# Kernel optimization log

Measured on AMD Instinct MI355X. Metric: run time of the kernel, lower is better.

The kernel has to match this reference:

```python
import jax, jax.numpy as jnp
import numpy as np

N = 500_000   # total nodes
B = 4096      # number of graphs (segments)
D = 256       # feature dim (input_dim)
H = 4         # attention heads


def setup_inputs() -> dict:
    key = jax.random.key(0)
    ks = jax.random.split(key, 9)
    x = jax.random.normal(ks[0], (N, D), dtype=jnp.float32)
    membership = jnp.sort(jax.random.randint(ks[1], (N,), 0, B, dtype=jnp.int32))
    # xavier-normal-ish attention weight, shape (1, H, D//H)
    att_w = jax.random.normal(ks[2], (1, H, D // H), dtype=jnp.float32) * np.float32(np.sqrt(2.0 / (1 + D // H)))
    s = np.float32(1.0 / np.sqrt(D))
    gru_w_ih = jax.random.uniform(ks[3], (3 * D, D), minval=-s, maxval=s, dtype=jnp.float32)
    gru_w_hh = jax.random.uniform(ks[4], (3 * D, D), minval=-s, maxval=s, dtype=jnp.float32)
    gru_b_ih = jax.random.uniform(ks[5], (3 * D,), minval=-s, maxval=s, dtype=jnp.float32)
    gru_b_hh = jax.random.uniform(ks[6], (3 * D,), minval=-s, maxval=s, dtype=jnp.float32)
    sm = np.float32(1.0 / np.sqrt(4 * D))
    merge_w = jax.random.uniform(ks[7], (D, 4 * D), minval=-sm, maxval=sm, dtype=jnp.float32)
    merge_b = jax.random.uniform(ks[8], (D,), minval=-sm, maxval=sm, dtype=jnp.float32)
    return {"x": x, "membership": membership, "att_w": att_w,
            "gru_w_ih": gru_w_ih, "gru_w_hh": gru_w_hh,
            "gru_b_ih": gru_b_ih, "gru_b_hh": gru_b_hh,
            "merge_w": merge_w, "merge_b": merge_b}


def _readout(x, seg, att_w, gru_w_ih, gru_w_hh, gru_b_ih, gru_b_hh, merge_w, merge_b):
    n, d = x.shape
    # ---- branch 0: 'rnn-sum-max' (GRUCell on pseudo-nodes) ----
    h = jax.nn.gelu(x, approximate=False)                       # exact gelu as torch F.gelu
    center = jax.ops.segment_sum(h, seg, num_segments=B)        # op_center = 'sum'  (B, D)
    neighbor = jax.ops.segment_max(h, seg, num_segments=B)      # op_neighbor = 'max' (B, D)
    gi = center @ gru_w_ih.T + gru_b_ih                          # (B, 3D)
    gh = neighbor @ gru_w_hh.T + gru_b_hh                        # (B, 3D)
    i_r, i_z, i_n = jnp.split(gi, 3, axis=-1)
    h_r, h_z, h_n = jnp.split(gh, 3, axis=-1)
    r = jax.nn.sigmoid(i_r + h_r)
    z = jax.nn.sigmoid(i_z + h_z)
    ng = jnp.tanh(i_n + r * h_n)
    rnn_out = (1.0 - z) * ng + z * neighbor                      # (B, D)
    # ---- branch 1: 'att' (single mode, segment softmax) ----
    xv = x.reshape(n, H, d // H)
    alpha = jax.nn.leaky_relu(jnp.sum(xv * att_w, axis=-1), negative_slope=0.2)  # (N, H)
    amax = jax.ops.segment_max(alpha, seg, num_segments=B)       # (B, H)
    e = jnp.exp(alpha - amax[seg])
    denom = jax.ops.segment_sum(e, seg, num_segments=B)
    a = e / denom[seg]                                           # segment softmax (N, H)
    att_out = jax.ops.segment_sum((xv * a[:, :, None]).reshape(n, d), seg, num_segments=B)
    # ---- branch 2/3: 'max', 'sum' ----
    max_out = jax.ops.segment_max(x, seg, num_segments=B)
    sum_out = jax.ops.segment_sum(x, seg, num_segments=B)
    # ---- merge: cat + Linear ----
    merged = jnp.concatenate([rnn_out, att_out, max_out, sum_out], axis=-1)  # (B, 4D)
    return merged @ merge_w.T + merge_b                          # (B, D)


def reference(x, membership, att_w, gru_w_ih, gru_w_hh, gru_b_ih, gru_b_hh, merge_w, merge_b):
    return _readout(x, membership, att_w, gru_w_ih, gru_w_hh, gru_b_ih, gru_b_hh, merge_w, merge_b)
```

## Files before the change

### kernel.cpp

```cpp
#include <hip/hip_runtime.h>
#include <math.h>
#include <stdint.h>

#define NN 500000
#define NB 4096
#define DD 256
#define NBND 1954
#define WPREP 640

typedef short  short8  __attribute__((ext_vector_type(8)));
typedef short  short4v __attribute__((ext_vector_type(4)));
typedef float  floatx4 __attribute__((ext_vector_type(4)));
typedef float  f2      __attribute__((ext_vector_type(2)));

__device__ __forceinline__ f2 sp(float v) { return (f2){v, v}; }

__device__ __forceinline__ short f2bf(float f) {
    uint32_t u = __float_as_uint(f);
    u += 0x7fffu + ((u >> 16) & 1u);
    return (short)(u >> 16);
}
__device__ __forceinline__ float bf2f(short s) {
    uint32_t u = ((uint32_t)(unsigned short)s) << 16;
    return __uint_as_float(u);
}

__device__ __forceinline__ f2 gelu2(f2 x) {
    f2 z = __builtin_elementwise_abs(x) * sp(0.70710678118654752440f);
    f2 p = __builtin_elementwise_fma(z, sp(0.0000430638f), sp(0.0002765672f));
    p = __builtin_elementwise_fma(p, z, sp(0.0001520143f));
    p = __builtin_elementwise_fma(p, z, sp(0.0092705272f));
    p = __builtin_elementwise_fma(p, z, sp(0.0422820123f));
    p = __builtin_elementwise_fma(p, z, sp(0.0705230784f));
    p = __builtin_elementwise_fma(p, z, sp(1.0f));
    p = p * p; p = p * p; p = p * p; p = p * p;
    f2 r = { __builtin_amdgcn_rcpf(p.x), __builtin_amdgcn_rcpf(p.y) };
    f2 er = __builtin_elementwise_copysign(sp(1.0f) - r, x);
    return sp(0.5f) * x * (sp(1.0f) + er);
}

__global__ __launch_bounds__(256) void prep_kernel(
    const int*   __restrict__ seg,
    const float* __restrict__ w_ih,
    const float* __restrict__ w_hh,
    const float* __restrict__ merge_w,
    int*   __restrict__ bnd,
    short* __restrict__ wih_bf,
    short* __restrict__ whh_bf,
    short* __restrict__ mw_bf)
{
    const int bid = blockIdx.x;
    const int t   = threadIdx.x;
    if (bid < NBND) {
        int i = bid * 256 + t;
        if (i >= NN) return;
        int s = seg[i];
        if (i == 0) {
            for (int b = 0; b <= s; ++b) bnd[b] = 0;
        } else {
            int p = seg[i - 1];
            for (int b = p + 1; b <= s; ++b) bnd[b] = i;
        }
        if (i == NN - 1) {
            for (int b = s + 1; b <= NB; ++b) bnd[b] = NN;
        }
    } else {
        int base = (bid - NBND) * 1024 + t * 4;
        const float* src; short* dst;
        if (base < 196608)      { src = &w_ih[base];            dst = &wih_bf[base]; }
        else if (base < 393216) { src = &w_hh[base - 196608];   dst = &whh_bf[base - 196608]; }
        else                    { src = &merge_w[base - 393216]; dst = &mw_bf[base - 393216]; }
        float4 v = *(const float4*)src;
        *(short4v*)dst = (short4v){ f2bf(v.x), f2bf(v.y), f2bf(v.z), f2bf(v.w) };
    }
}

__global__ __launch_bounds__(256, 8) void seg_kernel(
    const float* __restrict__ x,
    const int*   __restrict__ bnd,
    const float* __restrict__ att_w,
    short* __restrict__ merged_bf,
    short* __restrict__ center_bf,
    short* __restrict__ neighbor_bf)
{
    const int b   = blockIdx.x;
    const int tid = threadIdx.x;
    const int w   = tid >> 6;
    const int l   = tid & 63;

    const int start = bnd[b];
    const int end   = bnd[b + 1];

    const int cnt = end - start;
    const int q = cnt >> 2, r = cnt & 3;
    const int my_start = start + w * q + (w < r ? w : r);
    const int my_cnt   = q + (w < r ? 1 : 0);

    const float4 awv = *reinterpret_cast<const float4*>(&att_w[4 * l]);
    const f2 aw01 = {awv.x, awv.y}, aw23 = {awv.z, awv.w};

    f2 c01 = sp(0.f), c23 = sp(0.f);
    f2 s01 = sp(0.f), s23 = sp(0.f);
    f2 m01 = sp(-INFINITY), m23 = sp(-INFINITY);
    f2 a01 = sp(0.f), a23 = sp(0.f);
    float lsum = 0.f;

    auto process = [&](const float4& v) {
        f2 vl = {v.x, v.y}, vh = {v.z, v.w};
        f2 gl = gelu2(vl), gh = gelu2(vh);
        c01 += gl; c23 += gh;
        s01 += vl; s23 += vh;
        m01 = __builtin_elementwise_max(m01, vl);
        m23 = __builtin_elementwise_max(m23, vh);
        f2 tp = __builtin_elementwise_fma(vh, aw23, vl * aw01);
        float t = tp.x + tp.y;
        t += __shfl_xor(t, 1, 64);
        t += __shfl_xor(t, 2, 64);
        t += __shfl_xor(t, 4, 64);
        t += __shfl_xor(t, 8, 64);
        float alpha = fmaxf(t, 0.2f * t);
        float e = __expf(alpha);
        lsum += e;
        f2 ev = sp(e);
        a01 = __builtin_elementwise_fma(ev, vl, a01);
        a23 = __builtin_elementwise_fma(ev, vh, a23);
    };

    const float* __restrict__ xl = x + 4 * l;
    auto LD = [&](int row) -> float4 {
        int rc = row < (NN - 1) ? row : (NN - 1);
        return *reinterpret_cast<const float4*>(&xl[(size_t)rc * DD]);
    };

    float4 q0 = LD(my_start),     q1 = LD(my_start + 1),
           q2 = LD(my_start + 2), q3 = LD(my_start + 3);
    int ip = my_start + 4;
    int rem = my_cnt;
    while (rem >= 2) {
        float4 f0 = LD(ip), f1 = LD(ip + 1);
        process(q0); process(q1);
        q0 = q2; q1 = q3; q2 = f0; q3 = f1;
        ip += 2; rem -= 2;
    }
    if (rem) process(q0);

    __shared__ float lds[4][4][256];
    __shared__ float ldsl[4][4];
    const int c = 4 * l;
    lds[0][w][c+0] = c01.x; lds[0][w][c+1] = c01.y; lds[0][w][c+2] = c23.x; lds[0][w][c+3] = c23.y;
    lds[1][w][c+0] = s01.x; lds[1][w][c+1] = s01.y; lds[1][w][c+2] = s23.x; lds[1][w][c+3] = s23.y;
    lds[2][w][c+0] = m01.x; lds[2][w][c+1] = m01.y; lds[2][w][c+2] = m23.x; lds[2][w][c+3] = m23.y;
    lds[3][w][c+0] = a01.x; lds[3][w][c+1] = a01.y; lds[3][w][c+2] = a23.x; lds[3][w][c+3] = a23.y;
    if ((l & 15) == 0) ldsl[w][l >> 4] = lsum;
    __syncthreads();

    const int d = tid;
    float cs = lds[0][0][d] + lds[0][1][d] + lds[0][2][d] + lds[0][3][d];
    float ss = lds[1][0][d] + lds[1][1][d] + lds[1][2][d] + lds[1][3][d];
    float mm = fmaxf(fmaxf(lds[2][0][d], lds[2][1][d]), fmaxf(lds[2][2][d], lds[2][3][d]));
    float ac = lds[3][0][d] + lds[3][1][d] + lds[3][2][d] + lds[3][3][d];
    const int h = d >> 6;
    float denom = ldsl[0][h] + ldsl[1][h] + ldsl[2][h] + ldsl[3][h];
    float att = (denom > 0.f) ? ac / denom : 0.f;
    float nm = gelu2((f2){mm, mm}).x;

    short* mrow = merged_bf + (size_t)b * 1024;
    mrow[256 + d] = f2bf(att);
    mrow[512 + d] = f2bf(mm);
    mrow[768 + d] = f2bf(ss);
    center_bf  [(size_t)b * DD + d] = f2bf(cs);
    neighbor_bf[(size_t)b * DD + d] = f2bf(nm);
}

__global__ __launch_bounds__(256) void gru_and_basemerge(
    const short* __restrict__ center_bf,
    const short* __restrict__ neighbor_bf,
    const short* __restrict__ wih_bf,
    const short* __restrict__ whh_bf,
    const float* __restrict__ b_ih,
    const float* __restrict__ b_hh,
    short* __restrict__ merged_bf,
    const short* __restrict__ mw_bf,
    const float* __restrict__ merge_b,
    float* __restrict__ out)
{
    __shared__ short smem[16128];
    const int t   = threadIdx.x;
    const int w   = t >> 6, l = t & 63;
    const int l15 = l & 15, lq = l >> 4;

    if (blockIdx.x < 1024) {
        short* Ac = smem;
        short* An = smem + 4608;
        short* Wt = smem + 9216;

        const int m0 = (blockIdx.x >> 4) * 64;
        const int j0 = (blockIdx.x & 15) * 16;
        const int lr = t >> 2;
        const int lc = (t & 3) * 16;

        int wg[3], wrow[3], wk8[3];
        const short* wbase[3];
        #pragma unroll
        for (int i = 0; i < 3; ++i) {
            int f = i * 256 + t;
            wg[i]  = f >> 7;
            int idx = f & 127;
            wrow[i] = idx >> 3;
            wk8[i]  = (idx & 7) * 8;
            wbase[i] = (wg[i] < 3)
                ? &wih_bf[(size_t)(wg[i] * 256 + j0 + wrow[i]) * 256 + wk8[i]]
                : &whh_bf[(size_t)((wg[i] - 3) * 256 + j0 + wrow[i]) * 256 + wk8[i]];
        }
        const short* crp = &center_bf  [(size_t)(m0 + lr) * 256 + lc];
        const short* nrp = &neighbor_bf[(size_t)(m0 + lr) * 256 + lc];

        floatx4 acc[6] = {};

        short8 c0 = *(const short8*)(crp), c1 = *(const short8*)(crp + 8);
        short8 n0 = *(const short8*)(nrp), n1 = *(const short8*)(nrp + 8);
        short8 wv0 = *(const short8*)(wbase[0]);
        short8 wv1 = *(const short8*)(wbase[1]);
        short8 wv2 = *(const short8*)(wbase[2]);

        for (int k0 = 0; k0 < 256; k0 += 64) {
            const int kn = (k0 + 64 < 256) ? k0 + 64 : k0;
            short8 nc0 = *(const short8*)(crp + kn), nc1 = *(const short8*)(crp + kn + 8);
            short8 nn0 = *(const short8*)(nrp + kn), nn1 = *(const short8*)(nrp + kn + 8);
            short8 nw0 = *(const short8*)(wbase[0] + kn);
            short8 nw1 = *(const short8*)(wbase[1] + kn);
            short8 nw2 = *(const short8*)(wbase[2] + kn);

            __syncthreads();
            *(short8*)&Ac[lr * 72 + lc]     = c0;
            *(short8*)&Ac[lr * 72 + lc + 8] = c1;
            *(short8*)&An[lr * 72 + lc]     = n0;
            *(short8*)&An[lr * 72 + lc + 8] = n1;
            *(short8*)&Wt[wg[0] * 1152 + wrow[0] * 72 + wk8[0]] = wv0;
            *(short8*)&Wt[wg[1] * 1152 + wrow[1] * 72 + wk8[1]] = wv1;
            *(short8*)&Wt[wg[2] * 1152 + wrow[2] * 72 + wk8[2]] = wv2;
            __syncthreads();

            short8 afc[2], afn[2];
            #pragma unroll
            for (int ks = 0; ks < 2; ++ks) {
                afc[ks] = *(short8*)&Ac[(w * 16 + l15) * 72 + ks * 32 + lq * 8];
                afn[ks] = *(short8*)&An[(w * 16 + l15) * 72 + ks * 32 + lq * 8];
            }
            #pragma unroll
            for (int gg = 0; gg < 6; ++gg) {
                #pragma unroll
                for (int ks = 0; ks < 2; ++ks) {
                    short8 bf = *(short8*)&Wt[gg * 1152 + l15 * 72 + ks * 32 + lq * 8];
                    acc[gg] = __builtin_amdgcn_mfma_f32_16x16x32_bf16(
                        (gg < 3) ? afc[ks] : afn[ks], bf, acc[gg], 0, 0, 0);
                }
            }

            c0 = nc0; c1 = nc1; n0 = nn0; n1 = nn1;
            wv0 = nw0; wv1 = nw1; wv2 = nw2;
        }

        const int col = j0 + l15;
        const float bir = b_ih[col], biz = b_ih[256 + col], bin = b_ih[512 + col];
        const float bhr = b_hh[col], bhz = b_hh[256 + col], bhn = b_hh[512 + col];
        #pragma unroll
        for (int qq = 0; qq < 4; ++qq) {
            const int row = m0 + w * 16 + lq * 4 + qq;
            float rr = 1.f / (1.f + __expf(-(acc[0][qq] + bir + acc[3][qq] + bhr)));
            float zz = 1.f / (1.f + __expf(-(acc[1][qq] + biz + acc[4][qq] + bhz)));
            float ng = tanhf(acc[2][qq] + bin + rr * (acc[5][qq] + bhn));
            float nb = bf2f(neighbor_bf[(size_t)row * 256 + col]);
            merged_bf[(size_t)row * 1024 + col] = f2bf((1.f - zz) * ng + zz * nb);
        }
    } else {
        short* As = smem;
        short* Bs = smem + 4608;

        const int bid2 = blockIdx.x - 1024;
        const int m0 = (bid2 & 63) * 64, n0 = (bid2 >> 6) * 64;
        const int arow = t >> 2, ak = (t & 3) * 16;
        const int wm = w >> 1, wn = w & 1;

        const short* ap = &merged_bf[(size_t)(m0 + arow) * 1024 + 256 + ak];
        const short* bp = &mw_bf    [(size_t)(n0 + arow) * 1024 + 256 + ak];

        floatx4 acc[2][2] = {};

        short8 a0 = *(const short8*)(ap), a1 = *(const short8*)(ap + 8);
        short8 b0 = *(const short8*)(bp), b1 = *(const short8*)(bp + 8);

        for (int k0 = 0; k0 < 768; k0 += 64) {
            const int kn = (k0 + 64 < 768) ? k0 + 64 : k0;
            short8 na0 = *(const short8*)(ap + kn), na1 = *(const short8*)(ap + kn + 8);
            short8 nb0 = *(const short8*)(bp + kn), nb1 = *(const short8*)(bp + kn + 8);

            __syncthreads();
            *(short8*)&As[arow * 72 + ak]     = a0;
            *(short8*)&As[arow * 72 + ak + 8] = a1;
            *(short8*)&Bs[arow * 72 + ak]     = b0;
            *(short8*)&Bs[arow * 72 + ak + 8] = b1;
            __syncthreads();

            #pragma unroll
            for (int ks = 0; ks < 2; ++ks) {
                short8 af0 = *(short8*)&As[(wm * 32 +      l15) * 72 + ks * 32 + lq * 8];
                short8 af1 = *(short8*)&As[(wm * 32 + 16 + l15) * 72 + ks * 32 + lq * 8];
                short8 bf0 = *(short8*)&Bs[(wn * 32 +      l15) * 72 + ks * 32 + lq * 8];
                short8 bf1 = *(short8*)&Bs[(wn * 32 + 16 + l15) * 72 + ks * 32 + lq * 8];
                acc[0][0] = __builtin_amdgcn_mfma_f32_16x16x32_bf16(af0, bf0, acc[0][0], 0, 0, 0);
                acc[0][1] = __builtin_amdgcn_mfma_f32_16x16x32_bf16(af0, bf1, acc[0][1], 0, 0, 0);
                acc[1][0] = __builtin_amdgcn_mfma_f32_16x16x32_bf16(af1, bf0, acc[1][0], 0, 0, 0);
                acc[1][1] = __builtin_amdgcn_mfma_f32_16x16x32_bf16(af1, bf1, acc[1][1], 0, 0, 0);
            }

            a0 = na0; a1 = na1; b0 = nb0; b1 = nb1;
        }

        #pragma unroll
        for (int mi = 0; mi < 2; ++mi) {
            #pragma unroll
            for (int nj = 0; nj < 2; ++nj) {
                const int col = n0 + wn * 32 + 16 * nj + l15;
                const float bv = merge_b[col];
                #pragma unroll
                for (int qq = 0; qq < 4; ++qq) {
                    const int row = m0 + wm * 32 + 16 * mi + lq * 4 + qq;
                    out[(size_t)row * 256 + col] = acc[mi][nj][qq] + bv;
                }
            }
        }
    }
}

__global__ __launch_bounds__(256) void rnn_merge(
    const short* __restrict__ merged_bf,
    const short* __restrict__ mw_bf,
    float* __restrict__ out)
{
    __shared__ short As[64 * 72];
    __shared__ short Bs[64 * 72];

    const int t   = threadIdx.x;
    const int w   = t >> 6, l = t & 63;
    const int wm  = w >> 1, wn = w & 1;
    const int m0  = (blockIdx.x & 63) * 64, n0 = (blockIdx.x >> 6) * 64;
    const int arow = t >> 2, ak = (t & 3) * 16;
    const int l15 = l & 15, lq = l >> 4;

    const short* ap = &merged_bf[(size_t)(m0 + arow) * 1024 + ak];
    const short* bp = &mw_bf    [(size_t)(n0 + arow) * 1024 + ak];

    floatx4 acc[2][2] = {};

    short8 a0 = *(const short8*)(ap), a1 = *(const short8*)(ap + 8);
    short8 b0 = *(const short8*)(bp), b1 = *(const short8*)(bp + 8);

    for (int k0 = 0; k0 < 256; k0 += 64) {
        const int kn = (k0 + 64 < 256) ? k0 + 64 : k0;
        short8 na0 = *(const short8*)(ap + kn), na1 = *(const short8*)(ap + kn + 8);
        short8 nb0 = *(const short8*)(bp + kn), nb1 = *(const short8*)(bp + kn + 8);

        __syncthreads();
        *(short8*)&As[arow * 72 + ak]     = a0;
        *(short8*)&As[arow * 72 + ak + 8] = a1;
        *(short8*)&Bs[arow * 72 + ak]     = b0;
        *(short8*)&Bs[arow * 72 + ak + 8] = b1;
        __syncthreads();

        #pragma unroll
        for (int ks = 0; ks < 2; ++ks) {
            short8 af0 = *(short8*)&As[(wm * 32 +      l15) * 72 + ks * 32 + lq * 8];
            short8 af1 = *(short8*)&As[(wm * 32 + 16 + l15) * 72 + ks * 32 + lq * 8];
            short8 bf0 = *(short8*)&Bs[(wn * 32 +      l15) * 72 + ks * 32 + lq * 8];
            short8 bf1 = *(short8*)&Bs[(wn * 32 + 16 + l15) * 72 + ks * 32 + lq * 8];
            acc[0][0] = __builtin_amdgcn_mfma_f32_16x16x32_bf16(af0, bf0, acc[0][0], 0, 0, 0);
            acc[0][1] = __builtin_amdgcn_mfma_f32_16x16x32_bf16(af0, bf1, acc[0][1], 0, 0, 0);
            acc[1][0] = __builtin_amdgcn_mfma_f32_16x16x32_bf16(af1, bf0, acc[1][0], 0, 0, 0);
            acc[1][1] = __builtin_amdgcn_mfma_f32_16x16x32_bf16(af1, bf1, acc[1][1], 0, 0, 0);
        }

        a0 = na0; a1 = na1; b0 = nb0; b1 = nb1;
    }

    #pragma unroll
    for (int mi = 0; mi < 2; ++mi) {
        #pragma unroll
        for (int nj = 0; nj < 2; ++nj) {
            const int col = n0 + wn * 32 + 16 * nj + l15;
            #pragma unroll
            for (int qq = 0; qq < 4; ++qq) {
                const int row = m0 + wm * 32 + 16 * mi + lq * 4 + qq;
                out[(size_t)row * 256 + col] += acc[mi][nj][qq];
            }
        }
    }
}

extern "C" void kernel_launch(void* const* d_in, const int* in_sizes, int n_in,
                              void* d_out, int out_size, void* d_ws, size_t ws_size,
                              hipStream_t stream) {
    const float* x       = (const float*)d_in[0];
    const int*   seg     = (const int*)  d_in[1];
    const float* att_w   = (const float*)d_in[2];
    const float* w_ih    = (const float*)d_in[3];
    const float* w_hh    = (const float*)d_in[4];
    const float* b_ih    = (const float*)d_in[5];
    const float* b_hh    = (const float*)d_in[6];
    const float* merge_w = (const float*)d_in[7];
    const float* merge_b = (const float*)d_in[8];
    float* out = (float*)d_out;

    short* merged_bf   = (short*)d_ws;
    short* center_bf   = merged_bf   + (size_t)NB * 1024;
    short* neighbor_bf = center_bf   + (size_t)NB * DD;
    int*   bnd         = (int*)(neighbor_bf + (size_t)NB * DD);
    short* wih_bf      = (short*)(bnd + 8192);
    short* whh_bf      = wih_bf + 196608;
    short* mw_bf       = whh_bf + 196608;

    prep_kernel<<<NBND + WPREP, 256, 0, stream>>>(
        seg, w_ih, w_hh, merge_w, bnd, wih_bf, whh_bf, mw_bf);

    seg_kernel<<<NB, 256, 0, stream>>>(x, bnd, att_w, merged_bf, center_bf, neighbor_bf);

    gru_and_basemerge<<<1024 + 256, 256, 0, stream>>>(
        center_bf, neighbor_bf, wih_bf, whh_bf, b_ih, b_hh,
        merged_bf, mw_bf, merge_b, out);

    rnn_merge<<<256, 256, 0, stream>>>(merged_bf, mw_bf, out);
}
```

Before: 135.0 us.

## Move weight bf16 conversion into seg kernel and halve rnn_merge M-tile

The fp32-to-bf16 weight conversion blocks move out of the prep kernel and are appended as extra blocks to the segment reduction kernel, leaving a small boundary-only kernel in front. The conversion then overlaps with the bandwidth-heavy segment pass and shortens the dependency chain before it. Separately, the rnn_merge GEMM tile shrinks from 64x64 to 32x64, doubling the block count to 512 for better CU coverage on a small GEMM, at the cost of more B-tile reloads per output.

```diff
diff --git a/kernel.cpp b/kernel.cpp
--- a/kernel.cpp
+++ b/kernel.cpp
@@ -39,52 +39,51 @@
     return sp(0.5f) * x * (sp(1.0f) + er);
 }
 
-__global__ __launch_bounds__(256) void prep_kernel(
-    const int*   __restrict__ seg,
+__global__ __launch_bounds__(256) void seg_bounds(
+    const int* __restrict__ seg, int* __restrict__ bnd)
+{
+    int i = blockIdx.x * 256 + threadIdx.x;
+    if (i >= NN) return;
+    int s = seg[i];
+    if (i == 0) {
+        for (int b = 0; b <= s; ++b) bnd[b] = 0;
+    } else {
+        int p = seg[i - 1];
+        for (int b = p + 1; b <= s; ++b) bnd[b] = i;
+    }
+    if (i == NN - 1) {
+        for (int b = s + 1; b <= NB; ++b) bnd[b] = NN;
+    }
+}
+
+__global__ __launch_bounds__(256, 8) void seg_kernel(
+    const float* __restrict__ x,
+    const int*   __restrict__ bnd,
+    const float* __restrict__ att_w,
     const float* __restrict__ w_ih,
     const float* __restrict__ w_hh,
     const float* __restrict__ merge_w,
-    int*   __restrict__ bnd,
+    short* __restrict__ merged_bf,
+    short* __restrict__ center_bf,
+    short* __restrict__ neighbor_bf,
     short* __restrict__ wih_bf,
     short* __restrict__ whh_bf,
     short* __restrict__ mw_bf)
 {
-    const int bid = blockIdx.x;
-    const int t   = threadIdx.x;
-    if (bid < NBND) {
-        int i = bid * 256 + t;
-        if (i >= NN) return;
-        int s = seg[i];
-        if (i == 0) {
-            for (int b = 0; b <= s; ++b) bnd[b] = 0;
-        } else {
-            int p = seg[i - 1];
-            for (int b = p + 1; b <= s; ++b) bnd[b] = i;
-        }
-        if (i == NN - 1) {
-            for (int b = s + 1; b <= NB; ++b) bnd[b] = NN;
-        }
-    } else {
-        int base = (bid - NBND) * 1024 + t * 4;
+    const int tid = threadIdx.x;
+
+    if (blockIdx.x >= NB) {
+        int base = (blockIdx.x - NB) * 1024 + tid * 4;
         const float* src; short* dst;
-        if (base < 196608)      { src = &w_ih[base];            dst = &wih_bf[base]; }
-        else if (base < 393216) { src = &w_hh[base - 196608];   dst = &whh_bf[base - 196608]; }
+        if (base < 196608)      { src = &w_ih[base];             dst = &wih_bf[base]; }
+        else if (base < 393216) { src = &w_hh[base - 196608];    dst = &whh_bf[base - 196608]; }
         else                    { src = &merge_w[base - 393216]; dst = &mw_bf[base - 393216]; }
         float4 v = *(const float4*)src;
         *(short4v*)dst = (short4v){ f2bf(v.x), f2bf(v.y), f2bf(v.z), f2bf(v.w) };
-    }
-}
-
-__global__ __launch_bounds__(256, 8) void seg_kernel(
-    const float* __restrict__ x,
-    const int*   __restrict__ bnd,
-    const float* __restrict__ att_w,
-    short* __restrict__ merged_bf,
-    short* __restrict__ center_bf,
-    short* __restrict__ neighbor_bf)
-{
+        return;
+    }
+
     const int b   = blockIdx.x;
-    const int tid = threadIdx.x;
     const int w   = tid >> 6;
     const int l   = tid & 63;
 
@@ -338,61 +337,55 @@
     const short* __restrict__ mw_bf,
     float* __restrict__ out)
 {
-    __shared__ short As[64 * 72];
+    __shared__ short As[32 * 72];
     __shared__ short Bs[64 * 72];
 
     const int t   = threadIdx.x;
     const int w   = t >> 6, l = t & 63;
     const int wm  = w >> 1, wn = w & 1;
-    const int m0  = (blockIdx.x & 63) * 64, n0 = (blockIdx.x >> 6) * 64;
-    const int arow = t >> 2, ak = (t & 3) * 16;
+    const int m0  = (blockIdx.x & 127) * 32, n0 = (blockIdx.x >> 7) * 64;
+    const int arow = t >> 3, ak = (t & 7) * 8;
+    const int brow = t >> 2, bk = (t & 3) * 16;
     const int l15 = l & 15, lq = l >> 4;
 
     const short* ap = &merged_bf[(size_t)(m0 + arow) * 1024 + ak];
-    const short* bp = &mw_bf    [(size_t)(n0 + arow) * 1024 + ak];
-
-    floatx4 acc[2][2] = {};
-
-    short8 a0 = *(const short8*)(ap), a1 = *(const short8*)(ap + 8);
+    const short* bp = &mw_bf    [(size_t)(n0 + brow) * 1024 + bk];
+
+    floatx4 acc[2] = {};
+
+    short8 a0 = *(const short8*)(ap);
     short8 b0 = *(const short8*)(bp), b1 = *(const short8*)(bp + 8);
 
     for (int k0 = 0; k0 < 256; k0 += 64) {
         const int kn = (k0 + 64 < 256) ? k0 + 64 : k0;
-        short8 na0 = *(const short8*)(ap + kn), na1 = *(const short8*)(ap + kn + 8);
+        short8 na0 = *(const short8*)(ap + kn);
         short8 nb0 = *(const short8*)(bp + kn), nb1 = *(const short8*)(bp + kn + 8);
 
         __syncthreads();
-        *(short8*)&As[arow * 72 + ak]     = a0;
-        *(short8*)&As[arow * 72 + ak + 8] = a1;
-        *(short8*)&Bs[arow * 72 + ak]     = b0;
-        *(short8*)&Bs[arow * 72 + ak + 8] = b1;
+        *(short8*)&As[arow * 72 + ak]    = a0;
+        *(short8*)&Bs[brow * 72 + bk]    = b0;
+        *(short8*)&Bs[brow * 72 + bk + 8] = b1;
         __syncthreads();
 
         #pragma unroll
         for (int ks = 0; ks < 2; ++ks) {
-            short8 af0 = *(short8*)&As[(wm * 32 +      l15) * 72 + ks * 32 + lq * 8];
-            short8 af1 = *(short8*)&As[(wm * 32 + 16 + l15) * 72 + ks * 32 + lq * 8];
+            short8 af  = *(short8*)&As[(wm * 16 + l15) * 72 + ks * 32 + lq * 8];
             short8 bf0 = *(short8*)&Bs[(wn * 32 +      l15) * 72 + ks * 32 + lq * 8];
             short8 bf1 = *(short8*)&Bs[(wn * 32 + 16 + l15) * 72 + ks * 32 + lq * 8];
-            acc[0][0] = __builtin_amdgcn_mfma_f32_16x16x32_bf16(af0, bf0, acc[0][0], 0, 0, 0);
-            acc[0][1] = __builtin_amdgcn_mfma_f32_16x16x32_bf16(af0, bf1, acc[0][1], 0, 0, 0);
-            acc[1][0] = __builtin_amdgcn_mfma_f32_16x16x32_bf16(af1, bf0, acc[1][0], 0, 0, 0);
-            acc[1][1] = __builtin_amdgcn_mfma_f32_16x16x32_bf16(af1, bf1, acc[1][1], 0, 0, 0);
-        }
-
-        a0 = na0; a1 = na1; b0 = nb0; b1 = nb1;
+            acc[0] = __builtin_amdgcn_mfma_f32_16x16x32_bf16(af, bf0, acc[0], 0, 0, 0);
+            acc[1] = __builtin_amdgcn_mfma_f32_16x16x32_bf16(af, bf1, acc[1], 0, 0, 0);
+        }
+
+        a0 = na0; b0 = nb0; b1 = nb1;
     }
 
     #pragma unroll
-    for (int mi = 0; mi < 2; ++mi) {
+    for (int nj = 0; nj < 2; ++nj) {
+        const int col = n0 + wn * 32 + 16 * nj + l15;
         #pragma unroll
-        for (int nj = 0; nj < 2; ++nj) {
-            const int col = n0 + wn * 32 + 16 * nj + l15;
-            #pragma unroll
-            for (int qq = 0; qq < 4; ++qq) {
-                const int row = m0 + wm * 32 + 16 * mi + lq * 4 + qq;
-                out[(size_t)row * 256 + col] += acc[mi][nj][qq];
-            }
+        for (int qq = 0; qq < 4; ++qq) {
+            const int row = m0 + wm * 16 + lq * 4 + qq;
+            out[(size_t)row * 256 + col] += acc[nj][qq];
         }
     }
 }
@@ -419,14 +412,15 @@
     short* whh_bf      = wih_bf + 196608;
     short* mw_bf       = whh_bf + 196608;
 
-    prep_kernel<<<NBND + WPREP, 256, 0, stream>>>(
-        seg, w_ih, w_hh, merge_w, bnd, wih_bf, whh_bf, mw_bf);
-
-    seg_kernel<<<NB, 256, 0, stream>>>(x, bnd, att_w, merged_bf, center_bf, neighbor_bf);
+    seg_bounds<<<NBND, 256, 0, stream>>>(seg, bnd);
+
+    seg_kernel<<<NB + WPREP, 256, 0, stream>>>(
+        x, bnd, att_w, w_ih, w_hh, merge_w,
+        merged_bf, center_bf, neighbor_bf, wih_bf, whh_bf, mw_bf);
 
     gru_and_basemerge<<<1024 + 256, 256, 0, stream>>>(
         center_bf, neighbor_bf, wih_bf, whh_bf, b_ih, b_hh,
         merged_bf, mw_bf, merge_b, out);
 
-    rnn_merge<<<256, 256, 0, stream>>>(merged_bf, mw_bf, out);
-}
+    rnn_merge<<<512, 256, 0, stream>>>(merged_bf, mw_bf, out);
+}
```

New measurement: 133.3 us. Within noise of the previous version (-1.3%).
